# Kernel optimization log

Hardware: AMD Instinct MI355X
Metric: run time of the kernel (lower is better)

## Reference

```python
import jax, jax.numpy as jnp
import numpy as np

B, S, HID, NH, HD = 2, 2048, 1024, 16, 64


def setup_inputs() -> dict:
    key = jax.random.key(0)
    k0, k1, k2, k3 = jax.random.split(key, 4)
    scale = 1.0 / np.sqrt(HID)
    return {
        "x": jax.random.normal(k0, (B, S, HID), dtype=jnp.float32),
        "wq": jax.random.normal(k1, (HID, HID), dtype=jnp.float32) * scale,
        "wk": jax.random.normal(k2, (HID, HID), dtype=jnp.float32) * scale,
        "wv": jax.random.normal(k3, (HID, HID), dtype=jnp.float32) * scale,
    }


def reference(x, wq, wk, wv):
    b, s, _ = x.shape
    # nn.Linear(bias=False): y = x @ W^T ; reshape to [B, H, S, D]
    q = (x @ wq.T).reshape(b, s, NH, HD).transpose(0, 2, 1, 3)
    k = (x @ wk.T).reshape(b, s, NH, HD).transpose(0, 2, 1, 3)
    v = (x @ wv.T).reshape(b, s, NH, HD).transpose(0, 2, 1, 3)
    att = jnp.einsum("bhqd,bhkd->bhqk", q, k) / np.sqrt(HD)
    score = jax.nn.softmax(att.astype(jnp.float32), axis=-1)  # dropout p=0.0 -> identity
    attv = jnp.einsum("bhqk,bhkd->bhqd", score, v)  # [B, H, S, D]
    # faithful to original bug: .view(B, S, -1) on contiguous [B,H,S,D] WITHOUT transpose back
    attv = attv.reshape(b, s, NH * HD)
    return score, attv
```

## Files before the change

### kernel.cpp

```cpp
#include <hip/hip_runtime.h>
#include <hip/hip_bf16.h>
#include <stdint.h>
#include <stddef.h>

#define NB 2
#define SEQ 2048
#define HIDN 1024
#define NHEAD 16
#define HDIM 64
#define MTOT (NB * SEQ)

typedef short bf16x8 __attribute__((ext_vector_type(8)));
typedef _Float16 f16x8 __attribute__((ext_vector_type(8)));
typedef __fp16 h16x2 __attribute__((ext_vector_type(2)));
typedef float f32x4 __attribute__((ext_vector_type(4)));
typedef uint32_t u32x4 __attribute__((ext_vector_type(4)));

#define MFMA16(a, b, c)  __builtin_amdgcn_mfma_f32_16x16x32_bf16(a, b, c, 0, 0, 0)
#define MFMAH16(a, b, c) __builtin_amdgcn_mfma_f32_16x16x32_f16(a, b, c, 0, 0, 0)

__device__ __forceinline__ unsigned short f2bf(float f) {
  union { float f; uint32_t u; } v; v.f = f;
  uint32_t u = v.u;
  uint32_t r = (u + 0x7fffu + ((u >> 16) & 1u)) >> 16;
  return (unsigned short)r;
}

__device__ __forceinline__ unsigned short f2h(float f) {
  _Float16 h = (_Float16)f;
  return *reinterpret_cast<unsigned short*>(&h);
}

__device__ __forceinline__ float h2f(unsigned short u) {
  _Float16 h = *reinterpret_cast<_Float16*>(&u);
  return (float)h;
}

__device__ __forceinline__ void gload16(const void* g, void* l) {
  __builtin_amdgcn_global_load_lds((const __attribute__((address_space(1))) void*)g,
                                   (__attribute__((address_space(3))) void*)l,
                                   16, 0, 0);
}

__global__ void cvt_bf16(const float* __restrict__ x, const float* __restrict__ wq,
                         const float* __restrict__ wk, const float* __restrict__ wv,
                         unsigned short* __restrict__ dst)
{
  size_t i4 = ((size_t)blockIdx.x * blockDim.x + threadIdx.x) * 4;
  const float* s; size_t off;
  if (i4 < 4194304UL)      { s = x;  off = i4; }
  else if (i4 < 5242880UL) { s = wq; off = i4 - 4194304UL; }
  else if (i4 < 6291456UL) { s = wk; off = i4 - 5242880UL; }
  else                     { s = wv; off = i4 - 6291456UL; }
  float4 v = *(const float4*)(s + off);
  ushort4 o;
  o.x = f2bf(v.x); o.y = f2bf(v.y); o.z = f2bf(v.z); o.w = f2bf(v.w);
  *(ushort4*)(dst + i4) = o;
}

__global__ __launch_bounds__(256, 3) void qkv_gemm(
    const unsigned short* __restrict__ xb,
    const unsigned short* __restrict__ wqb,
    const unsigned short* __restrict__ wkb,
    const unsigned short* __restrict__ wvb,
    unsigned short* __restrict__ Qb,
    unsigned short* __restrict__ Kb,
    unsigned short* __restrict__ Vt)
{
  __shared__ unsigned short As[128 * 64];
  __shared__ unsigned short Bs[128 * 64];

  const int z = blockIdx.z;
  const unsigned short* W = (z == 0) ? wqb : (z == 1) ? wkb : wvb;
  const int n0 = blockIdx.x * 128;
  const int m0 = blockIdx.y * 128;
  const int tid = threadIdx.x;
  const int lane = tid & 63;
  const int wid = tid >> 6;
  const int l15 = lane & 15;
  const int lg = lane >> 4;

  f32x4 acc[4][4] = {};

  const int wr = (wid >> 1) * 64;
  const int wc = (wid & 1) * 64;

  for (int kt = 0; kt < 16; ++kt) {
    __syncthreads();
    #pragma unroll
    for (int i = 0; i < 4; ++i) {
      int row = wid * 32 + i * 8 + (lane >> 3);
      int chunk = (lane & 7) ^ (row & 7);
      const unsigned short* ga = xb + (size_t)(m0 + row) * HIDN + kt * 64 + chunk * 8;
      const unsigned short* gb = W  + (size_t)(n0 + row) * HIDN + kt * 64 + chunk * 8;
      gload16(ga, (char*)As + wid * 4096 + i * 1024);
      gload16(gb, (char*)Bs + wid * 4096 + i * 1024);
    }
    __syncthreads();

    #pragma unroll
    for (int ks = 0; ks < 2; ++ks) {
      bf16x8 af[4], bfr[4];
      #pragma unroll
      for (int mi = 0; mi < 4; ++mi) {
        int row = wr + mi * 16 + l15;
        int cb = (ks * 64 + lg * 16) ^ ((row & 7) << 4);
        af[mi] = *(const bf16x8*)((const char*)As + row * 128 + cb);
      }
      #pragma unroll
      for (int ni = 0; ni < 4; ++ni) {
        int row = wc + ni * 16 + l15;
        int cb = (ks * 64 + lg * 16) ^ ((row & 7) << 4);
        bfr[ni] = *(const bf16x8*)((const char*)Bs + row * 128 + cb);
      }
      #pragma unroll
      for (int mi = 0; mi < 4; ++mi)
        #pragma unroll
        for (int ni = 0; ni < 4; ++ni)
          acc[mi][ni] = MFMA16(af[mi], bfr[ni], acc[mi][ni]);
    }
  }

  if (z < 2) {
    unsigned short* O = (z == 0) ? Qb : Kb;
    #pragma unroll
    for (int mi = 0; mi < 4; ++mi)
      #pragma unroll
      for (int ni = 0; ni < 4; ++ni) {
        int n = n0 + wc + ni * 16 + l15;
        #pragma unroll
        for (int e = 0; e < 4; ++e) {
          int m = m0 + wr + mi * 16 + lg * 4 + e;
          if (z == 0) {
            O[(size_t)m * HIDN + n] = f2bf(acc[mi][ni][e]);
          } else {
            int mm = (m & ~31) | (((m >> 2) & 1) << 4) | (((m >> 3) & 3) << 2) | (m & 3);
            int nn = (n & ~56) | (((((n >> 3) & 7) ^ (mm & 7))) << 3);
            O[(size_t)mm * HIDN + nn] = f2bf(acc[mi][ni][e]);
          }
        }
      }
  } else {
    #pragma unroll
    for (int mi = 0; mi < 4; ++mi)
      #pragma unroll
      for (int ni = 0; ni < 4; ++ni) {
        int n = n0 + wc + ni * 16 + l15;
        int m = m0 + wr + mi * 16 + lg * 4;
        int mmv = (m & ~120) | (((((m >> 3) & 15) ^ (n & 15))) << 3);
        ushort4 pk;
        pk.x = f2h(acc[mi][ni][0]);
        pk.y = f2h(acc[mi][ni][1]);
        pk.z = f2h(acc[mi][ni][2]);
        pk.w = f2h(acc[mi][ni][3]);
        *(ushort4*)(Vt + (size_t)n * MTOT + mmv) = pk;
      }
  }
}

__global__ __launch_bounds__(512, 4) void attn_pv(
    const unsigned short* __restrict__ Qb,
    const unsigned short* __restrict__ Kb,
    const unsigned short* __restrict__ Vt,
    float* __restrict__ invs,
    float* __restrict__ out)
{
  __shared__ unsigned short Ks[2][128 * 64];
  __shared__ unsigned short Vs[2][64 * 128];

  const int bid = blockIdx.x;
  const int xcd = bid & 7;
  const int rest = bid >> 3;
  const int pan = (rest & 3) * 8 + xcd;
  const int slab = rest >> 2;
  const int b = pan >> 4, h = pan & 15;
  const int tid = threadIdx.x;
  const int wid = tid >> 6;
  const int lane = tid & 63;
  const int l15 = lane & 15, lg = lane >> 4;
  const int q0 = slab * 128 + wid * 16;

  const unsigned short* qptr = Qb + ((size_t)(b * SEQ + q0 + l15) * HIDN + h * HDIM + lg * 8);
  const bf16x8 bq0 = *(const bf16x8*)qptr;
  const bf16x8 bq1 = *(const bf16x8*)(qptr + 32);

  const float C = 0.18033688011112042f;

  const unsigned short* kpanel = Kb + (size_t)b * SEQ * HIDN + h * HDIM;
  const unsigned short* vpanel = Vt + (size_t)h * HDIM * MTOT + b * SEQ;

  #define STAGE_K(buf, c) { \
    _Pragma("unroll") \
    for (int i = 0; i < 2; ++i) { \
      int row = wid * 8 + i * 64 + (lane >> 3); \
      const unsigned short* src = kpanel + (size_t)((c) * 128 + row) * HIDN + (lane & 7) * 8; \
      gload16(src, (char*)Ks[buf] + wid * 1024 + i * 8192); \
    } }
  #define STAGE_V(buf, c) { \
    _Pragma("unroll") \
    for (int i = 0; i < 2; ++i) { \
      int dl = wid * 4 + i * 32 + (lane >> 4); \
      const unsigned short* src = vpanel + (size_t)dl * MTOT + (c) * 128 + (lane & 15) * 8; \
      gload16(src, (char*)Vs[buf] + wid * 1024 + i * 8192); \
    } }

  STAGE_K(0, 0); STAGE_V(0, 0);
  __builtin_amdgcn_sched_barrier(0);
  asm volatile("s_waitcnt vmcnt(0)" ::: "memory");
  __builtin_amdgcn_s_barrier();
  __builtin_amdgcn_sched_barrier(0);

  float sm = 0.f;
  f32x4 pv[4] = {};

  for (int c = 0; c < 16; ++c) {
    const int cur = c & 1;
    if (c < 15) { STAGE_K(cur ^ 1, c + 1); STAGE_V(cur ^ 1, c + 1); }
    __builtin_amdgcn_sched_barrier(0);

    f32x4 acc[8] = {};
    #pragma unroll
    for (int kf = 0; kf < 8; ++kf) {
      const int rowL = kf * 16 + l15;
      const char* kr = (const char*)Ks[cur] + rowL * 128;
      bf16x8 a0 = *(const bf16x8*)(kr + ((lg    ) ^ (rowL & 7)) * 16);
      bf16x8 a1 = *(const bf16x8*)(kr + ((lg + 4) ^ (rowL & 7)) * 16);
      acc[kf] = MFMA16(a0, bq0, acc[kf]);
      acc[kf] = MFMA16(a1, bq1, acc[kf]);
    }

    #pragma unroll
    for (int t = 0; t < 4; ++t) {
      float4 s0, s1;
      s0.x = exp2f(acc[2 * t][0] * C);
      s0.y = exp2f(acc[2 * t][1] * C);
      s0.z = exp2f(acc[2 * t][2] * C);
      s0.w = exp2f(acc[2 * t][3] * C);
      s1.x = exp2f(acc[2 * t + 1][0] * C);
      s1.y = exp2f(acc[2 * t + 1][1] * C);
      s1.z = exp2f(acc[2 * t + 1][2] * C);
      s1.w = exp2f(acc[2 * t + 1][3] * C);
      sm += ((s0.x + s0.y) + (s0.z + s0.w)) + ((s1.x + s1.y) + (s1.z + s1.w));

      union PKu { h16x2 h2[4]; f16x8 h8; } pk;
      pk.h2[0] = __builtin_amdgcn_cvt_pkrtz(s0.x, s0.y);
      pk.h2[1] = __builtin_amdgcn_cvt_pkrtz(s0.z, s0.w);
      pk.h2[2] = __builtin_amdgcn_cvt_pkrtz(s1.x, s1.y);
      pk.h2[3] = __builtin_amdgcn_cvt_pkrtz(s1.z, s1.w);

      #pragma unroll
      for (int nf = 0; nf < 4; ++nf) {
        const int d = nf * 16 + l15;
        f16x8 bv = *(const f16x8*)((const char*)Vs[cur] + d * 256 + (((t * 4 + lg) ^ l15)) * 16);
        pv[nf] = MFMAH16(pk.h8, bv, pv[nf]);
      }
    }

    __builtin_amdgcn_sched_barrier(0);
    asm volatile("s_waitcnt vmcnt(0)" ::: "memory");
    __builtin_amdgcn_s_barrier();
    __builtin_amdgcn_sched_barrier(0);
  }

  #pragma unroll
  for (int off = 16; off <= 32; off <<= 1) sm += __shfl_xor(sm, off, 64);
  const float inv = __builtin_amdgcn_rcpf(sm);
  if (lane < 16) invs[(size_t)(b * NHEAD + h) * SEQ + q0 + lane] = inv;

  float* av = out + (size_t)NB * NHEAD * SEQ * SEQ
            + ((size_t)(b * NHEAD + h) * SEQ + q0 + 4 * lg) * HDIM + l15;
  #pragma unroll
  for (int e = 0; e < 4; ++e) {
    const float invq = __shfl(inv, 4 * lg + e, 64);
    #pragma unroll
    for (int nf = 0; nf < 4; ++nf)
      __builtin_nontemporal_store(pv[nf][e] * invq, av + (size_t)e * HDIM + nf * 16);
  }
  #undef STAGE_K
  #undef STAGE_V
}

__global__ __launch_bounds__(512, 2) void score_emit(
    const unsigned short* __restrict__ Qb,
    const unsigned short* __restrict__ Kb,
    const float* __restrict__ invs,
    float* __restrict__ out)
{
  __shared__ unsigned short P[16 * 2048];

  const int bid = blockIdx.x;
  const int xcd = bid & 7;
  const int rest = bid >> 3;
  const int pan = (rest & 3) * 8 + xcd;
  const int blkp = rest >> 2;
  const int b = pan >> 4, h = pan & 15;
  const int tid = threadIdx.x;
  const int wid = tid >> 6;
  const int lane = tid & 63;
  const int l15 = lane & 15, lg = lane >> 4;

  const float C = 0.18033688011112042f;
  const unsigned short* kpanel = Kb + (size_t)b * SEQ * HIDN + h * HDIM;
  const size_t panrow0 = (size_t)(b * NHEAD + h) * SEQ;

  for (int tt = 0; tt < 8; ++tt) {
    const int q0 = (blkp * 8 + tt) * 16;

    const unsigned short* qptr = Qb + ((size_t)(b * SEQ + q0 + l15) * HIDN + h * HDIM + lg * 8);
    const bf16x8 bq0 = *(const bf16x8*)qptr;
    const bf16x8 bq1 = *(const bf16x8*)(qptr + 32);

    #pragma unroll
    for (int i = 0; i < 2; ++i) {
      const int c = wid * 2 + i;
      f32x4 acc[8] = {};
      #pragma unroll
      for (int kf = 0; kf < 8; ++kf) {
        const int s = c * 128 + kf * 16 + l15;
        const unsigned short* kr = kpanel + (size_t)s * HIDN;
        bf16x8 a0 = *(const bf16x8*)(kr + ((lg      ^ (s & 7))) * 8);
        bf16x8 a1 = *(const bf16x8*)(kr + (((lg + 4) ^ (s & 7))) * 8);
        acc[kf] = MFMA16(a0, bq0, acc[kf]);
        acc[kf] = MFMA16(a1, bq1, acc[kf]);
      }
      #pragma unroll
      for (int t = 0; t < 4; ++t) {
        float4 s0, s1;
        s0.x = exp2f(acc[2 * t][0] * C);
        s0.y = exp2f(acc[2 * t][1] * C);
        s0.z = exp2f(acc[2 * t][2] * C);
        s0.w = exp2f(acc[2 * t][3] * C);
        s1.x = exp2f(acc[2 * t + 1][0] * C);
        s1.y = exp2f(acc[2 * t + 1][1] * C);
        s1.z = exp2f(acc[2 * t + 1][2] * C);
        s1.w = exp2f(acc[2 * t + 1][3] * C);

        union PKu { h16x2 h2[4]; u32x4 u4; } pk;
        pk.h2[0] = __builtin_amdgcn_cvt_pkrtz(s0.x, s0.y);
        pk.h2[1] = __builtin_amdgcn_cvt_pkrtz(s0.z, s0.w);
        pk.h2[2] = __builtin_amdgcn_cvt_pkrtz(s1.x, s1.y);
        pk.h2[3] = __builtin_amdgcn_cvt_pkrtz(s1.z, s1.w);

        const int off = c * 256 + ((((t * 4 + lg) ^ l15)) << 4);
        *(u32x4*)((char*)P + l15 * 4096 + off) = pk.u4;
      }
    }

    asm volatile("s_waitcnt lgkmcnt(0)" ::: "memory");
    __builtin_amdgcn_s_barrier();
    __builtin_amdgcn_sched_barrier(0);

    #pragma unroll
    for (int i = 0; i < 2; ++i) {
      const int r = wid * 2 + i;
      const float invr = invs[panrow0 + q0 + r];
      float* orow = out + (panrow0 + q0 + r) * SEQ;
      #pragma unroll
      for (int g = 0; g < 8; ++g) {
        const int o = g * 512 + lane * 8;
        const int ph = o ^ ((r & 15) << 4);
        uint2 w = *(const uint2*)((const char*)P + r * 4096 + ph);
        f32x4 ov;
        ov[0] = h2f((unsigned short)(w.x & 0xffff)) * invr;
        ov[1] = h2f((unsigned short)(w.x >> 16)) * invr;
        ov[2] = h2f((unsigned short)(w.y & 0xffff)) * invr;
        ov[3] = h2f((unsigned short)(w.y >> 16)) * invr;
        __builtin_nontemporal_store(ov, (f32x4*)(orow + (o >> 1)));
      }
    }

    asm volatile("s_waitcnt lgkmcnt(0)" ::: "memory");
    __builtin_amdgcn_s_barrier();
    __builtin_amdgcn_sched_barrier(0);
  }
}

extern "C" void kernel_launch(void* const* d_in, const int* in_sizes, int n_in,
                              void* d_out, int out_size, void* d_ws, size_t ws_size,
                              hipStream_t stream)
{
  const float* x  = (const float*)d_in[0];
  const float* wq = (const float*)d_in[1];
  const float* wk = (const float*)d_in[2];
  const float* wv = (const float*)d_in[3];
  float* out = (float*)d_out;
  unsigned short* ws = (unsigned short*)d_ws;

  unsigned short* xb  = ws;
  unsigned short* wqb = ws + 4194304;
  unsigned short* wkb = ws + 5242880;
  unsigned short* wvb = ws + 6291456;
  unsigned short* Qb  = ws + 7340032;
  unsigned short* Kb  = ws + 11534336;
  unsigned short* Vt  = ws + 15728640;
  float* invs = (float*)ws;

  cvt_bf16<<<7168, 256, 0, stream>>>(x, wq, wk, wv, ws);
  qkv_gemm<<<dim3(8, 32, 3), 256, 0, stream>>>(xb, wqb, wkb, wvb, Qb, Kb, Vt);
  attn_pv<<<512, 512, 0, stream>>>(Qb, Kb, Vt, invs, out);
  score_emit<<<512, 512, 0, stream>>>(Qb, Kb, invs, out);
}
```

Baseline: 194.6 us.

## Fuse Q, K and V projections into one GEMM kernel sharing the x tile

Replaces the three-way z-indexed QKV GEMM launch with a single kernel. Each 512-thread block loads one x tile and all three weight tiles, then computes the Q, K and V outputs with per-wave 32x64 subtiles. This removes the repeated reads of the x tile across the three projections and cuts the launch to 256 blocks. In exchange, LDS use per block rises to about 64KB, there is one block per CU with fewer independent blocks, and accumulator register pressure goes up.

```diff
diff --git a/kernel.cpp b/kernel.cpp
--- a/kernel.cpp
+++ b/kernel.cpp
@@ -58,7 +58,7 @@
   *(ushort4*)(dst + i4) = o;
 }
 
-__global__ __launch_bounds__(256, 3) void qkv_gemm(
+__global__ __launch_bounds__(512, 2) void qkv_fused(
     const unsigned short* __restrict__ xb,
     const unsigned short* __restrict__ wqb,
     const unsigned short* __restrict__ wkb,
@@ -68,10 +68,8 @@
     unsigned short* __restrict__ Vt)
 {
   __shared__ unsigned short As[128 * 64];
-  __shared__ unsigned short Bs[128 * 64];
-
-  const int z = blockIdx.z;
-  const unsigned short* W = (z == 0) ? wqb : (z == 1) ? wkb : wvb;
+  __shared__ unsigned short Bs[3][128 * 64];
+
   const int n0 = blockIdx.x * 128;
   const int m0 = blockIdx.y * 128;
   const int tid = threadIdx.x;
@@ -80,82 +78,100 @@
   const int l15 = lane & 15;
   const int lg = lane >> 4;
 
-  f32x4 acc[4][4] = {};
-
-  const int wr = (wid >> 1) * 64;
+  const unsigned short* Wz[3] = { wqb, wkb, wvb };
+
+  f32x4 acc[3][2][4] = {};
+
+  const int wr = (wid >> 1) * 32;
   const int wc = (wid & 1) * 64;
 
   for (int kt = 0; kt < 16; ++kt) {
     __syncthreads();
     #pragma unroll
-    for (int i = 0; i < 4; ++i) {
-      int row = wid * 32 + i * 8 + (lane >> 3);
-      int chunk = (lane & 7) ^ (row & 7);
-      const unsigned short* ga = xb + (size_t)(m0 + row) * HIDN + kt * 64 + chunk * 8;
-      const unsigned short* gb = W  + (size_t)(n0 + row) * HIDN + kt * 64 + chunk * 8;
-      gload16(ga, (char*)As + wid * 4096 + i * 1024);
-      gload16(gb, (char*)Bs + wid * 4096 + i * 1024);
-    }
+    for (int i = 0; i < 2; ++i) {
+      const int idx = i * 512 + tid;
+      const int row = idx >> 3;
+      const int chunk = (idx & 7) ^ (row & 7);
+      gload16(xb + (size_t)(m0 + row) * HIDN + kt * 64 + chunk * 8,
+              (char*)As + (wid * 64 + (lane & 63)) * 0 + idx * 16 - lane * 16 + lane * 16);
+    }
+    #pragma unroll
+    for (int z = 0; z < 3; ++z)
+      #pragma unroll
+      for (int i = 0; i < 2; ++i) {
+        const int idx = i * 512 + tid;
+        const int row = idx >> 3;
+        const int chunk = (idx & 7) ^ (row & 7);
+        gload16(Wz[z] + (size_t)(n0 + row) * HIDN + kt * 64 + chunk * 8,
+                (char*)Bs[z] + idx * 16);
+      }
     __syncthreads();
 
     #pragma unroll
     for (int ks = 0; ks < 2; ++ks) {
-      bf16x8 af[4], bfr[4];
-      #pragma unroll
-      for (int mi = 0; mi < 4; ++mi) {
+      bf16x8 af[2];
+      #pragma unroll
+      for (int mi = 0; mi < 2; ++mi) {
         int row = wr + mi * 16 + l15;
         int cb = (ks * 64 + lg * 16) ^ ((row & 7) << 4);
         af[mi] = *(const bf16x8*)((const char*)As + row * 128 + cb);
       }
       #pragma unroll
-      for (int ni = 0; ni < 4; ++ni) {
-        int row = wc + ni * 16 + l15;
-        int cb = (ks * 64 + lg * 16) ^ ((row & 7) << 4);
-        bfr[ni] = *(const bf16x8*)((const char*)Bs + row * 128 + cb);
-      }
-      #pragma unroll
-      for (int mi = 0; mi < 4; ++mi)
+      for (int z = 0; z < 3; ++z) {
+        bf16x8 bfr[4];
         #pragma unroll
-        for (int ni = 0; ni < 4; ++ni)
-          acc[mi][ni] = MFMA16(af[mi], bfr[ni], acc[mi][ni]);
+        for (int ni = 0; ni < 4; ++ni) {
+          int row = wc + ni * 16 + l15;
+          int cb = (ks * 64 + lg * 16) ^ ((row & 7) << 4);
+          bfr[ni] = *(const bf16x8*)((const char*)Bs[z] + row * 128 + cb);
+        }
+        #pragma unroll
+        for (int mi = 0; mi < 2; ++mi)
+          #pragma unroll
+          for (int ni = 0; ni < 4; ++ni)
+            acc[z][mi][ni] = MFMA16(af[mi], bfr[ni], acc[z][mi][ni]);
+      }
     }
   }
 
-  if (z < 2) {
-    unsigned short* O = (z == 0) ? Qb : Kb;
-    #pragma unroll
-    for (int mi = 0; mi < 4; ++mi)
-      #pragma unroll
-      for (int ni = 0; ni < 4; ++ni) {
-        int n = n0 + wc + ni * 16 + l15;
-        #pragma unroll
-        for (int e = 0; e < 4; ++e) {
-          int m = m0 + wr + mi * 16 + lg * 4 + e;
-          if (z == 0) {
-            O[(size_t)m * HIDN + n] = f2bf(acc[mi][ni][e]);
-          } else {
-            int mm = (m & ~31) | (((m >> 2) & 1) << 4) | (((m >> 3) & 3) << 2) | (m & 3);
-            int nn = (n & ~56) | (((((n >> 3) & 7) ^ (mm & 7))) << 3);
-            O[(size_t)mm * HIDN + nn] = f2bf(acc[mi][ni][e]);
-          }
-        }
-      }
-  } else {
-    #pragma unroll
-    for (int mi = 0; mi < 4; ++mi)
-      #pragma unroll
-      for (int ni = 0; ni < 4; ++ni) {
-        int n = n0 + wc + ni * 16 + l15;
-        int m = m0 + wr + mi * 16 + lg * 4;
-        int mmv = (m & ~120) | (((((m >> 3) & 15) ^ (n & 15))) << 3);
-        ushort4 pk;
-        pk.x = f2h(acc[mi][ni][0]);
-        pk.y = f2h(acc[mi][ni][1]);
-        pk.z = f2h(acc[mi][ni][2]);
-        pk.w = f2h(acc[mi][ni][3]);
-        *(ushort4*)(Vt + (size_t)n * MTOT + mmv) = pk;
-      }
-  }
+  #pragma unroll
+  for (int mi = 0; mi < 2; ++mi)
+    #pragma unroll
+    for (int ni = 0; ni < 4; ++ni) {
+      int n = n0 + wc + ni * 16 + l15;
+      #pragma unroll
+      for (int e = 0; e < 4; ++e) {
+        int m = m0 + wr + mi * 16 + lg * 4 + e;
+        Qb[(size_t)m * HIDN + n] = f2bf(acc[0][mi][ni][e]);
+      }
+    }
+  #pragma unroll
+  for (int mi = 0; mi < 2; ++mi)
+    #pragma unroll
+    for (int ni = 0; ni < 4; ++ni) {
+      int n = n0 + wc + ni * 16 + l15;
+      #pragma unroll
+      for (int e = 0; e < 4; ++e) {
+        int m = m0 + wr + mi * 16 + lg * 4 + e;
+        int mm = (m & ~31) | (((m >> 2) & 1) << 4) | (((m >> 3) & 3) << 2) | (m & 3);
+        int nn = (n & ~56) | (((((n >> 3) & 7) ^ (mm & 7))) << 3);
+        Kb[(size_t)mm * HIDN + nn] = f2bf(acc[1][mi][ni][e]);
+      }
+    }
+  #pragma unroll
+  for (int mi = 0; mi < 2; ++mi)
+    #pragma unroll
+    for (int ni = 0; ni < 4; ++ni) {
+      int n = n0 + wc + ni * 16 + l15;
+      int m = m0 + wr + mi * 16 + lg * 4;
+      int mmv = (m & ~120) | (((((m >> 3) & 15) ^ (n & 15))) << 3);
+      ushort4 pk;
+      pk.x = f2h(acc[2][mi][ni][0]);
+      pk.y = f2h(acc[2][mi][ni][1]);
+      pk.z = f2h(acc[2][mi][ni][2]);
+      pk.w = f2h(acc[2][mi][ni][3]);
+      *(ushort4*)(Vt + (size_t)n * MTOT + mmv) = pk;
+    }
 }
 
 __global__ __launch_bounds__(512, 4) void attn_pv(
@@ -396,7 +412,7 @@
   float* invs = (float*)ws;
 
   cvt_bf16<<<7168, 256, 0, stream>>>(x, wq, wk, wv, ws);
-  qkv_gemm<<<dim3(8, 32, 3), 256, 0, stream>>>(xb, wqb, wkb, wvb, Qb, Kb, Vt);
+  qkv_fused<<<dim3(8, 32), 512, 0, stream>>>(xb, wqb, wkb, wvb, Qb, Kb, Vt);
   attn_pv<<<512, 512, 0, stream>>>(Qb, Kb, Vt, invs, out);
   score_emit<<<512, 512, 0, stream>>>(Qb, Kb, invs, out);
 }
```

Result: slower. 198.5 us (+2.0%).
